# Performance work log

Measured on AMD Instinct MI355X. Metric: run time of the kernel, lower is better.

## Reference

```python
import jax, jax.numpy as jnp
import numpy as np

B, N, D = 16, 1369, 1024
HID, NH = 512, 8
SCALE = np.sqrt(D // NH)


def _pos_encoding_2d(n, d):
    ps = int(np.sqrt(n))  # 37; n is a perfect square here
    div = jnp.exp(jnp.arange(0, d // 2, 2, dtype=jnp.float32) * (-np.log(10000.0) / (d // 2)))
    rows = (jnp.arange(n) // ps).astype(jnp.float32)
    cols = (jnp.arange(n) % ps).astype(jnp.float32)
    def interleave(s, c):
        return jnp.stack([s, c], axis=-1).reshape(n, -1)
    half_row = interleave(jnp.sin(rows[:, None] * div), jnp.cos(rows[:, None] * div))
    half_col = interleave(jnp.sin(cols[:, None] * div), jnp.cos(cols[:, None] * div))
    return jnp.concatenate([half_row, half_col], axis=-1)  # [n, d]


def _center_bias(n, strength=0.3):
    ps = int(np.sqrt(n))
    c = ps // 2
    y, x = jnp.meshgrid(jnp.arange(ps, dtype=jnp.float32), jnp.arange(ps, dtype=jnp.float32), indexing='ij')
    d2 = (x - c) ** 2 + (y - c) ** 2
    sigma = ps / 6.0
    return (jnp.exp(-d2 / (2.0 * sigma ** 2)).reshape(-1)) * strength  # [n]


def setup_inputs() -> dict:
    key = jax.random.key(0)
    ks = jax.random.split(key, 16)
    s = 0.02
    return {
        'patch_tokens': jax.random.normal(ks[0], (B, N, D), dtype=jnp.float32),
        'curiosity_score': jax.random.uniform(ks[1], (B,), dtype=jnp.float32),
        'Wq': jax.random.normal(ks[2], (D, D), dtype=jnp.float32) * s,
        'bq': jax.random.uniform(ks[3], (D,), minval=-0.05, maxval=0.05, dtype=jnp.float32),
        'Wk': jax.random.normal(ks[4], (D, D), dtype=jnp.float32) * s,
        'bk': jax.random.uniform(ks[5], (D,), minval=-0.05, maxval=0.05, dtype=jnp.float32),
        'Wv': jax.random.normal(ks[6], (D, D), dtype=jnp.float32) * s,
        'bv': jnp.zeros((D,), dtype=jnp.float32),
        'Wc1': jax.random.normal(ks[7], (1, HID // 8), dtype=jnp.float32) * s,
        'bc1': jnp.zeros((HID // 8,), dtype=jnp.float32),
        'Wc2': jax.random.normal(ks[8], (HID // 8, NH), dtype=jnp.float32) * s,
        'bc2': jnp.zeros((NH,), dtype=jnp.float32),
        'Wp1': jax.random.normal(ks[9], (D, HID), dtype=jnp.float32) * s,
        'bp1': jnp.zeros((HID,), dtype=jnp.float32),
        'Wp2': jax.random.normal(ks[10], (HID, HID // 4), dtype=jnp.float32) * s,
        'bp2': jnp.zeros((HID // 4,), dtype=jnp.float32),
        'adaptive_weight': jnp.float32(0.5),
    }


def reference(patch_tokens, curiosity_score, Wq, bq, Wk, bk, Wv, bv,
              Wc1, bc1, Wc2, bc2, Wp1, bp1, Wp2, bp2, adaptive_weight):
    b, n, d = patch_tokens.shape
    x = patch_tokens + _pos_encoding_2d(n, d)[None]  # [B,N,D]

    q = x @ Wq + bq
    k = x @ Wk + bk
    v = x @ Wv + bv

    scores = jnp.einsum('bqd,bkd->bqk', q, k) / SCALE          # [B,N,N]
    attn = jax.nn.softmax(scores, axis=-1)                     # dropout p=0 / eval
    attended = jnp.einsum('bqk,bkd->bqd', attn, v)             # [B,N,D]

    cb = _center_bias(n)[None]                                 # [1,N]
    VAR_EPS = 1e-6

    pa = attn.mean(axis=1) + cb
    # fallback chain (data-dependent in torch; expressed with jnp.where)
    pa2 = jnp.diagonal(attn, axis1=-2, axis2=-1) + cb
    pa = jnp.where(jnp.var(pa, ddof=1) < VAR_EPS, pa2, pa)
    pa3 = attn.max(axis=-1) + cb
    pa = jnp.where(jnp.var(pa, ddof=1) < VAR_EPS, pa3, pa)
    norms = jnp.linalg.norm(x, axis=-1)
    noise = jax.random.normal(jax.random.key(42), norms.shape, dtype=norms.dtype) * 0.1 * jnp.std(norms, ddof=1)
    pa = jnp.where(jnp.var(pa, ddof=1) < VAR_EPS, norms + noise, pa)

    pa = pa / (pa.sum(axis=-1, keepdims=True) + 1e-8)

    # curiosity modulation
    h = jax.nn.relu(curiosity_score[:, None] @ Wc1 + bc1)
    cm = jax.nn.sigmoid(h @ Wc2 + bc2)                         # [B,NH]
    cw = cm.mean(axis=-1, keepdims=True)                       # [B,1]
    modulated = pa * (1.0 + cw)
    fa = adaptive_weight * modulated + (1.0 - adaptive_weight) * pa

    fa = jnp.clip(fa, 1e-8, None)
    fa = fa / (fa.sum(axis=-1, keepdims=True) + 1e-8)

    weighted = jnp.sum(attended * fa[..., None], axis=1)       # [B,D]
    focal = jax.nn.relu(weighted @ Wp1 + bp1) @ Wp2 + bp2      # [B,HID//4]
    return focal, fa
```

## Files before the change

kernel.cpp:

```cpp
#include <hip/hip_runtime.h>
#include <hip/hip_bf16.h>
#include <cstdint>

#define B_   16
#define N_   1369
#define NP   1408
#define D_   1024

typedef __bf16 bf16x8_t __attribute__((ext_vector_type(8)));
typedef __bf16 bf16x4_t __attribute__((ext_vector_type(4)));
typedef float  f32x4_t  __attribute__((ext_vector_type(4)));

__device__ __forceinline__ float  bf2f(__bf16 x) { return (float)x; }
__device__ __forceinline__ __bf16 f2bf(float x)  { return (__bf16)x; }

#define GLOAD_LDS16(g, l) __builtin_amdgcn_global_load_lds( \
    (const __attribute__((address_space(1))) void*)(g),     \
    (__attribute__((address_space(3))) void*)(l), 16, 0, 0)

__global__ __launch_bounds__(256)
void pos_kernel(float* __restrict__ pos)
{
    const int idx = blockIdx.x * 256 + threadIdx.x;
    if (idx >= N_ * D_) return;
    const int n = idx >> 10, f = idx & 1023;
    const int row = n / 37, col = n - row * 37;
    const float base = (f < 512) ? (float)row : (float)col;
    const int  t2   = (f & 511) >> 1;
    const float dv  = __expf(-0.03597789207803197f * (float)t2);
    const float ang = base * dv;
    pos[idx] = (f & 1) ? cosf(ang) : sinf(ang);
}

__global__ __launch_bounds__(256)
void addpos_kernel(const float* __restrict__ patch, const float* __restrict__ pos,
                   __bf16* __restrict__ X)
{
    const long tid = (long)blockIdx.x * 256 + threadIdx.x;
    const long e   = tid * 4;
    const int  f   = (int)(e & 1023);
    const long nb  = e >> 10;
    const int  n   = (int)(nb % NP);
    const long b   = nb / NP;
    bf16x4_t o;
    if (n < N_) {
        const float4 p = *(const float4*)(patch + ((b * N_ + n) << 10) + f);
        const float4 q = *(const float4*)(pos + ((long)n << 10) + f);
        o[0] = f2bf(p.x + q.x); o[1] = f2bf(p.y + q.y);
        o[2] = f2bf(p.z + q.z); o[3] = f2bf(p.w + q.w);
    } else {
        o[0] = o[1] = o[2] = o[3] = f2bf(0.f);
    }
    *(bf16x4_t*)(X + e) = o;
}

__global__ __launch_bounds__(256)
void wcast_kernel(const float* __restrict__ W0, const float* __restrict__ W1,
                  const float* __restrict__ W2,
                  __bf16* __restrict__ T0, __bf16* __restrict__ T1, __bf16* __restrict__ T2)
{
    const float* W = blockIdx.z == 0 ? W0 : (blockIdx.z == 1 ? W1 : W2);
    __bf16*      T = blockIdx.z == 0 ? T0 : (blockIdx.z == 1 ? T1 : T2);
    __shared__ float tile[64][65];
    const int o0 = blockIdx.x * 64, i0 = blockIdx.y * 64;
    const int t = threadIdx.x;
    const int tr = t >> 4, tc = (t & 15) * 4;
    #pragma unroll
    for (int rr = 0; rr < 64; rr += 16) {
        float4 v = *(const float4*)(W + (long)(i0 + rr + tr) * 1024 + o0 + tc);
        tile[rr + tr][tc + 0] = v.x; tile[rr + tr][tc + 1] = v.y;
        tile[rr + tr][tc + 2] = v.z; tile[rr + tr][tc + 3] = v.w;
    }
    __syncthreads();
    #pragma unroll
    for (int rr = 0; rr < 64; rr += 16) {
        bf16x4_t o;
        o[0] = f2bf(tile[tc + 0][rr + tr]); o[1] = f2bf(tile[tc + 1][rr + tr]);
        o[2] = f2bf(tile[tc + 2][rr + tr]); o[3] = f2bf(tile[tc + 3][rr + tr]);
        *(bf16x4_t*)(T + (long)(o0 + rr + tr) * 1024 + i0 + tc) = o;
    }
}

template<int HAS_BIAS>
__global__ __launch_bounds__(256)
void gemm_tn(const __bf16* __restrict__ A, const __bf16* __restrict__ Bt,
             __bf16* __restrict__ C, const float* __restrict__ bias,
             int M, int Nn, int Kd, float scale,
             long sA, long sB, long sC)
{
    A  += (long)blockIdx.z * sA;
    Bt += (long)blockIdx.z * sB;
    C  += (long)blockIdx.z * sC;
    const int m0 = blockIdx.y * 128;
    const int n0 = blockIdx.x * 128;
    __shared__ __bf16 As[128 * 32];
    __shared__ __bf16 Bs[128 * 32];
    const int t = threadIdx.x;
    const int w = t >> 6, l = t & 63;
    const int wr = w >> 1, wc = w & 1;
    const int lr = l & 15, lh = l >> 4;

    f32x4_t acc[4][4] = {};

    const __bf16* aRd = As + (wr * 64 + lr) * 32 + lh * 8;
    const __bf16* bRd = Bs + (wc * 64 + lr) * 32 + lh * 8;

    const int L0 = w * 1024 + l * 16;
    const int r0 = L0 >> 6;
    const int e0 = (L0 & 63) >> 1;
    const __bf16* gA0 = A  + (long)(m0 + r0)      * Kd + e0;
    const __bf16* gA1 = A  + (long)(m0 + r0 + 64) * Kd + e0;
    const __bf16* gB0 = Bt + (long)(n0 + r0)      * Kd + e0;
    const __bf16* gB1 = Bt + (long)(n0 + r0 + 64) * Kd + e0;
    __bf16* lA0 = As + w * 512;
    __bf16* lA1 = As + 2048 + w * 512;
    __bf16* lB0 = Bs + w * 512;
    __bf16* lB1 = Bs + 2048 + w * 512;

    for (int k0 = 0; k0 < Kd; k0 += 32) {
        GLOAD_LDS16(gA0 + k0, lA0);
        GLOAD_LDS16(gA1 + k0, lA1);
        GLOAD_LDS16(gB0 + k0, lB0);
        GLOAD_LDS16(gB1 + k0, lB1);
        __syncthreads();
        bf16x8_t af[4], bfm[4];
        #pragma unroll
        for (int i = 0; i < 4; ++i) af[i]  = *(const bf16x8_t*)(aRd + i * 16 * 32);
        #pragma unroll
        for (int j = 0; j < 4; ++j) bfm[j] = *(const bf16x8_t*)(bRd + j * 16 * 32);
        #pragma unroll
        for (int i = 0; i < 4; ++i)
            #pragma unroll
            for (int j = 0; j < 4; ++j)
                acc[i][j] = __builtin_amdgcn_mfma_f32_16x16x32_bf16(af[i], bfm[j], acc[i][j], 0, 0, 0);
        __syncthreads();
    }

    #pragma unroll
    for (int i = 0; i < 4; ++i) {
        const int row = m0 + wr * 64 + i * 16 + lh * 4;
        #pragma unroll
        for (int j = 0; j < 4; ++j) {
            const int col = n0 + wc * 64 + j * 16 + lr;
            const float bb = HAS_BIAS ? bias[col] : 0.0f;
            #pragma unroll
            for (int q = 0; q < 4; ++q) {
                const float v = acc[i][j][q] * scale + bb;
                C[(long)(row + q) * Nn + col] = f2bf(v);
            }
        }
    }
}

__global__ __launch_bounds__(256)
void softmax_kernel(__bf16* __restrict__ S)
{
    const int q = blockIdx.x, b = blockIdx.y;
    __bf16* row = S + ((long)b * NP + q) * NP;
    const int t = threadIdx.x;
    float v[6];
    float m = -1e30f;
    #pragma unroll
    for (int i = 0; i < 6; ++i) {
        const int k = t + i * 256;
        float x = -1e30f;
        if (k < N_) x = bf2f(row[k]);
        v[i] = x;
        m = fmaxf(m, x);
    }
    __shared__ float red[8];
    #pragma unroll
    for (int o = 32; o; o >>= 1) m = fmaxf(m, __shfl_xor(m, o));
    if (!(t & 63)) red[t >> 6] = m;
    __syncthreads();
    m = fmaxf(fmaxf(red[0], red[1]), fmaxf(red[2], red[3]));
    float s = 0.f;
    #pragma unroll
    for (int i = 0; i < 6; ++i) {
        const int k = t + i * 256;
        if (k < N_) { const float e = __expf(v[i] - m); v[i] = e; s += e; }
    }
    #pragma unroll
    for (int o = 32; o; o >>= 1) s += __shfl_xor(s, o);
    if (!(t & 63)) red[4 + (t >> 6)] = s;
    __syncthreads();
    s = red[4] + red[5] + red[6] + red[7];
    const float inv = 1.f / s;
    #pragma unroll
    for (int i = 0; i < 6; ++i) {
        const int k = t + i * 256;
        if (k < N_)      row[k] = f2bf(v[i] * inv);
        else if (k < NP) row[k] = f2bf(0.f);
    }
}

template<int WEIGHTED>
__global__ __launch_bounds__(256)
void colsum_kernel(const __bf16* __restrict__ attn, const float* __restrict__ wv,
                   float* __restrict__ out)
{
    const int k = blockIdx.x * 256 + threadIdx.x;
    const int b = blockIdx.y;
    const int q0 = blockIdx.z * 172;
    const int q1 = (q0 + 172 < N_) ? q0 + 172 : N_;
    if (k >= N_) return;
    const __bf16* base = attn + (long)b * NP * NP + k;
    float s = 0.f;
    for (int q = q0; q < q1; ++q) {
        float a = bf2f(base[(long)q * NP]);
        if (WEIGHTED) a *= wv[b * NP + q];
        s += a;
    }
    atomicAdd(out + b * NP + k, s);
}

__global__ __launch_bounds__(256)
void fa_kernel(const float* __restrict__ pa_raw, const float* __restrict__ curiosity,
               const float* __restrict__ Wc1, const float* __restrict__ bc1,
               const float* __restrict__ Wc2, const float* __restrict__ bc2,
               const float* __restrict__ aw_p,
               float* __restrict__ fa_ws, float* __restrict__ out_fa)
{
    const int b = blockIdx.x, t = threadIdx.x;
    __shared__ float hsh[64];
    __shared__ float red[8];
    __shared__ float cwsh;
    if (t < 64) hsh[t] = fmaxf(0.f, curiosity[b] * Wc1[t] + bc1[t]);
    __syncthreads();
    if (t < 8) {
        float a = bc2[t];
        for (int j = 0; j < 64; ++j) a += hsh[j] * Wc2[j * 8 + t];
        red[t] = 1.f / (1.f + __expf(-a));
    }
    __syncthreads();
    if (t == 0) {
        float cw = 0.f;
        for (int i = 0; i < 8; ++i) cw += red[i];
        cwsh = cw * 0.125f;
    }
    __syncthreads();
    const float aw   = aw_p[0];
    const float modf = 1.f + aw * cwsh;
    const float sig  = 37.f / 6.f;
    const float inv2s2 = 1.f / (2.f * sig * sig);
    float pv[6];
    float s1 = 0.f;
    #pragma unroll
    for (int i = 0; i < 6; ++i) {
        const int k = t + i * 256;
        float p = 0.f;
        if (k < N_) {
            const int y = k / 37, x = k - y * 37;
            const float d2 = (float)((x - 18) * (x - 18) + (y - 18) * (y - 18));
            const float cb = 0.3f * __expf(-d2 * inv2s2);
            p = pa_raw[b * NP + k] * (1.f / 1369.f) + cb;
        }
        pv[i] = p; s1 += p;
    }
    #pragma unroll
    for (int o = 32; o; o >>= 1) s1 += __shfl_xor(s1, o);
    __syncthreads();
    if (!(t & 63)) red[t >> 6] = s1;
    __syncthreads();
    s1 = red[0] + red[1] + red[2] + red[3];
    const float inv1 = 1.f / (s1 + 1e-8f);
    float s2 = 0.f;
    #pragma unroll
    for (int i = 0; i < 6; ++i) {
        const int k = t + i * 256;
        if (k < N_) {
            const float f = fmaxf(pv[i] * inv1 * modf, 1e-8f);
            pv[i] = f; s2 += f;
        }
    }
    #pragma unroll
    for (int o = 32; o; o >>= 1) s2 += __shfl_xor(s2, o);
    if (!(t & 63)) red[4 + (t >> 6)] = s2;
    __syncthreads();
    s2 = red[4] + red[5] + red[6] + red[7];
    const float inv2 = 1.f / (s2 + 1e-8f);
    #pragma unroll
    for (int i = 0; i < 6; ++i) {
        const int k = t + i * 256;
        if (k < N_) {
            const float f = pv[i] * inv2;
            fa_ws[b * NP + k]  = f;
            out_fa[b * N_ + k] = f;
        }
    }
}

__global__ __launch_bounds__(256)
void weighted_kernel(const float* __restrict__ g, const __bf16* __restrict__ V,
                     float* __restrict__ wout)
{
    const int b  = blockIdx.y;
    const int k0 = blockIdx.x * 86;
    const int k1 = (k0 + 86 < N_) ? k0 + 86 : N_;
    const int d  = threadIdx.x * 4;
    float a0 = 0, a1 = 0, a2 = 0, a3 = 0;
    const __bf16* vb = V + (long)b * NP * D_ + d;
    for (int k = k0; k < k1; ++k) {
        const float gv = g[b * NP + k];
        bf16x4_t vv = *(const bf16x4_t*)(vb + (long)k * D_);
        a0 += gv * bf2f(vv[0]); a1 += gv * bf2f(vv[1]);
        a2 += gv * bf2f(vv[2]); a3 += gv * bf2f(vv[3]);
    }
    atomicAdd(wout + b * D_ + d + 0, a0);
    atomicAdd(wout + b * D_ + d + 1, a1);
    atomicAdd(wout + b * D_ + d + 2, a2);
    atomicAdd(wout + b * D_ + d + 3, a3);
}

__global__ __launch_bounds__(256)
void focal_kernel(const float* __restrict__ weighted, const float* __restrict__ Wp1,
                  const float* __restrict__ bp1, const float* __restrict__ Wp2,
                  const float* __restrict__ bp2, float* __restrict__ out)
{
    const int b = blockIdx.x, t = threadIdx.x;
    __shared__ float wsh[1024];
    __shared__ float hsh[512];
    for (int i = t; i < 1024; i += 256) wsh[i] = weighted[b * 1024 + i];
    __syncthreads();
    for (int j = t; j < 512; j += 256) {
        float a = bp1[j];
        for (int d2 = 0; d2 < 1024; ++d2) a += wsh[d2] * Wp1[d2 * 512 + j];
        hsh[j] = fmaxf(a, 0.f);
    }
    __syncthreads();
    for (int o = t; o < 128; o += 256) {
        float a = bp2[o];
        for (int j = 0; j < 512; ++j) a += hsh[j] * Wp2[j * 128 + o];
        out[b * 128 + o] = a;
    }
}

extern "C" void kernel_launch(void* const* d_in, const int* in_sizes, int n_in,
                              void* d_out, int out_size, void* d_ws, size_t ws_size,
                              hipStream_t stream)
{
    const float* patch     = (const float*)d_in[0];
    const float* curiosity = (const float*)d_in[1];
    const float* Wq  = (const float*)d_in[2];
    const float* bq  = (const float*)d_in[3];
    const float* Wk  = (const float*)d_in[4];
    const float* bk  = (const float*)d_in[5];
    const float* Wv  = (const float*)d_in[6];
    const float* bv  = (const float*)d_in[7];
    const float* Wc1 = (const float*)d_in[8];
    const float* bc1 = (const float*)d_in[9];
    const float* Wc2 = (const float*)d_in[10];
    const float* bc2 = (const float*)d_in[11];
    const float* Wp1 = (const float*)d_in[12];
    const float* bp1 = (const float*)d_in[13];
    const float* Wp2 = (const float*)d_in[14];
    const float* bp2 = (const float*)d_in[15];
    const float* aw  = (const float*)d_in[16];
    float* out = (float*)d_out;

    char* ws = (char*)d_ws;
    size_t off = 0;
    auto alloc = [&](size_t bytes) -> char* {
        char* p = ws + off;
        off += (bytes + 255) & ~(size_t)255;
        return p;
    };
    float*  pos  = (float*) alloc((size_t)N_ * D_ * 4);
    __bf16* X    = (__bf16*)alloc((size_t)B_ * NP * D_ * 2);
    __bf16* WqT  = (__bf16*)alloc((size_t)D_ * D_ * 2);
    __bf16* WkT  = (__bf16*)alloc((size_t)D_ * D_ * 2);
    __bf16* WvT  = (__bf16*)alloc((size_t)D_ * D_ * 2);
    __bf16* Q    = (__bf16*)alloc((size_t)B_ * NP * D_ * 2);
    __bf16* Kb   = (__bf16*)alloc((size_t)B_ * NP * D_ * 2);
    __bf16* V    = (__bf16*)alloc((size_t)B_ * NP * D_ * 2);
    __bf16* S    = (__bf16*)alloc((size_t)B_ * NP * NP * 2);
    float*  pa   = (float*) alloc((size_t)B_ * NP * 4);
    float*  faw  = (float*) alloc((size_t)B_ * NP * 4);
    float*  gbuf = (float*) alloc((size_t)B_ * NP * 4);
    float*  wsum = (float*) alloc((size_t)B_ * D_ * 4);

    (void)hipMemsetAsync(pa,   0, (size_t)B_ * NP * 4, stream);
    (void)hipMemsetAsync(gbuf, 0, (size_t)B_ * NP * 4, stream);
    (void)hipMemsetAsync(wsum, 0, (size_t)B_ * D_ * 4, stream);

    pos_kernel<<<(N_ * D_ + 255) / 256, 256, 0, stream>>>(pos);
    addpos_kernel<<<(int)((size_t)B_ * NP * D_ / 4 / 256), 256, 0, stream>>>(patch, pos, X);
    {
        dim3 g(16, 16, 3);
        wcast_kernel<<<g, 256, 0, stream>>>(Wq, Wk, Wv, WqT, WkT, WvT);
    }
    {
        dim3 g(D_ / 128, (B_ * NP) / 128, 1);
        gemm_tn<1><<<g, 256, 0, stream>>>(X, WqT, Q,  bq, B_ * NP, D_, D_, 1.f, 0, 0, 0);
        gemm_tn<1><<<g, 256, 0, stream>>>(X, WkT, Kb, bk, B_ * NP, D_, D_, 1.f, 0, 0, 0);
        gemm_tn<1><<<g, 256, 0, stream>>>(X, WvT, V,  bv, B_ * NP, D_, D_, 1.f, 0, 0, 0);
    }
    {
        dim3 g(NP / 128, NP / 128, B_);
        gemm_tn<0><<<g, 256, 0, stream>>>(Q, Kb, S, nullptr, NP, NP, D_,
                                          0.08838834764831845f,
                                          (long)NP * D_, (long)NP * D_, (long)NP * NP);
    }
    {
        dim3 g(N_, B_);
        softmax_kernel<<<g, 256, 0, stream>>>(S);
    }
    {
        dim3 g(6, B_, 8);
        colsum_kernel<0><<<g, 256, 0, stream>>>(S, nullptr, pa);
    }
    fa_kernel<<<B_, 256, 0, stream>>>(pa, curiosity, Wc1, bc1, Wc2, bc2, aw,
                                      faw, out + B_ * 128);
    {
        dim3 g(6, B_, 8);
        colsum_kernel<1><<<g, 256, 0, stream>>>(S, faw, gbuf);
    }
    {
        dim3 g(16, B_);
        weighted_kernel<<<g, 256, 0, stream>>>(gbuf, V, wsum);
    }
    focal_kernel<<<B_, 256, 0, stream>>>(wsum, Wp1, bp1, Wp2, bp2, out);
}
```

Baseline: 639.6 us.

## Fuse QKV projections into one 256x256 pipelined MFMA GEMM with swizzled LDS

```diff
diff --git a/kernel.cpp b/kernel.cpp
--- a/kernel.cpp
+++ b/kernel.cpp
@@ -4,8 +4,9 @@
 
 #define B_   16
 #define N_   1369
-#define NP   1408
+#define NP   1536
 #define D_   1024
+#define NQKV 3072
 
 typedef __bf16 bf16x8_t __attribute__((ext_vector_type(8)));
 typedef __bf16 bf16x4_t __attribute__((ext_vector_type(4)));
@@ -81,75 +82,125 @@
     }
 }
 
+__global__ __launch_bounds__(256)
+void bcat_kernel(const float* __restrict__ bq, const float* __restrict__ bk,
+                 const float* __restrict__ bv, float* __restrict__ bcat)
+{
+    const int i = blockIdx.x * 256 + threadIdx.x;
+    if (i >= NQKV) return;
+    const int p = i >> 10, j = i & 1023;
+    bcat[i] = p == 0 ? bq[j] : (p == 1 ? bk[j] : bv[j]);
+}
+
 template<int HAS_BIAS>
-__global__ __launch_bounds__(256)
-void gemm_tn(const __bf16* __restrict__ A, const __bf16* __restrict__ Bt,
+__global__ __launch_bounds__(512, 2)
+void gemm256(const __bf16* __restrict__ A, const __bf16* __restrict__ Bt,
              __bf16* __restrict__ C, const float* __restrict__ bias,
-             int M, int Nn, int Kd, float scale,
-             long sA, long sB, long sC)
-{
-    A  += (long)blockIdx.z * sA;
-    Bt += (long)blockIdx.z * sB;
-    C  += (long)blockIdx.z * sC;
-    const int m0 = blockIdx.y * 128;
-    const int n0 = blockIdx.x * 128;
-    __shared__ __bf16 As[128 * 32];
-    __shared__ __bf16 Bs[128 * 32];
-    const int t = threadIdx.x;
-    const int w = t >> 6, l = t & 63;
-    const int wr = w >> 1, wc = w & 1;
+             int lda, int ldb, int ldc, int Kd, float scale,
+             long sA, long sB, long sC, int tilesN, int tilesPerBatch, int cpx)
+{
+    __shared__ __bf16 lds[65536];
+    const int bid = blockIdx.x;
+    const int vt  = (bid & 7) * cpx + (bid >> 3);
+    const int bz  = vt / tilesPerBatch;
+    const int rem = vt - bz * tilesPerBatch;
+    const int ty  = rem / tilesN;
+    const int tx  = rem - ty * tilesN;
+    A  += (long)bz * sA;  Bt += (long)bz * sB;  C += (long)bz * sC;
+    const int m0 = ty * 256, n0 = tx * 256;
+
+    const int t  = threadIdx.x;
+    const int w  = t >> 6, l = t & 63;
+    const int wr = w >> 2, wc = w & 3;
     const int lr = l & 15, lh = l >> 4;
 
-    f32x4_t acc[4][4] = {};
-
-    const __bf16* aRd = As + (wr * 64 + lr) * 32 + lh * 8;
-    const __bf16* bRd = Bs + (wc * 64 + lr) * 32 + lh * 8;
-
-    const int L0 = w * 1024 + l * 16;
-    const int r0 = L0 >> 6;
-    const int e0 = (L0 & 63) >> 1;
-    const __bf16* gA0 = A  + (long)(m0 + r0)      * Kd + e0;
-    const __bf16* gA1 = A  + (long)(m0 + r0 + 64) * Kd + e0;
-    const __bf16* gB0 = Bt + (long)(n0 + r0)      * Kd + e0;
-    const __bf16* gB1 = Bt + (long)(n0 + r0 + 64) * Kd + e0;
-    __bf16* lA0 = As + w * 512;
-    __bf16* lA1 = As + 2048 + w * 512;
-    __bf16* lB0 = Bs + w * 512;
-    __bf16* lB1 = Bs + 2048 + w * 512;
-
-    for (int k0 = 0; k0 < Kd; k0 += 32) {
-        GLOAD_LDS16(gA0 + k0, lA0);
-        GLOAD_LDS16(gA1 + k0, lA1);
-        GLOAD_LDS16(gB0 + k0, lB0);
-        GLOAD_LDS16(gB1 + k0, lB1);
-        __syncthreads();
-        bf16x8_t af[4], bfm[4];
+    const int laneF  = (lr * 64 + ((lh * 16) ^ (((lr >> 3) & 1) << 5))) >> 1;
+    const int rstage = w * 16 + (l >> 2);
+    const int kstage = ((l & 3) * 8) ^ (((l >> 5) & 1) << 4);
+
+    const __bf16* Ag = A  + (long)(m0 + rstage) * lda + kstage;
+    const __bf16* Bg = Bt + (long)(n0 + rstage) * ldb + kstage;
+    __bf16* dA = lds + (w * 2) * 512;
+    __bf16* dB = lds + 16384 + (w * 2) * 512;
+
+#define SA_(buf, half, kt) do {                                       \
+    const __bf16* g_ = Ag + (long)(half) * 128 * lda + (kt) * 64;     \
+    __bf16* d_ = dA + (buf) * 32768 + (half) * 8192;                  \
+    GLOAD_LDS16(g_, d_); GLOAD_LDS16(g_ + 32, d_ + 512); } while (0)
+#define SB_(buf, half, kt) do {                                       \
+    const __bf16* g_ = Bg + (long)(half) * 128 * ldb + (kt) * 64;     \
+    __bf16* d_ = dB + (buf) * 32768 + (half) * 8192;                  \
+    GLOAD_LDS16(g_, d_); GLOAD_LDS16(g_ + 32, d_ + 512); } while (0)
+
+    f32x4_t acc[8][4] = {};
+    bf16x8_t bfr[4][2];
+
+#define BREADS_() do { const __bf16* bp_ = lds + cbB + laneF;                              \
+    bfr[0][0] = *(const bf16x8_t*)(bp_);        bfr[0][1] = *(const bf16x8_t*)(bp_ + 512); \
+    bfr[1][0] = *(const bf16x8_t*)(bp_ + 1024); bfr[1][1] = *(const bf16x8_t*)(bp_ + 1536);\
+    bfr[2][0] = *(const bf16x8_t*)(bp_ + 2048); bfr[2][1] = *(const bf16x8_t*)(bp_ + 2560);\
+    bfr[3][0] = *(const bf16x8_t*)(bp_ + 3072); bfr[3][1] = *(const bf16x8_t*)(bp_ + 3584);} while (0)
+
+#define PHASE_(p, P0R, STG, VMW) do {                                                  \
+    const __bf16* ap_ = lds + cbase + wr * 8192 + (p) * 2048 + laneF;                  \
+    bf16x8_t a00 = *(const bf16x8_t*)(ap_);                                            \
+    bf16x8_t a01 = *(const bf16x8_t*)(ap_ + 512);                                      \
+    bf16x8_t a10 = *(const bf16x8_t*)(ap_ + 1024);                                     \
+    bf16x8_t a11 = *(const bf16x8_t*)(ap_ + 1536);                                     \
+    P0R;                                                                               \
+    STG;                                                                               \
+    __builtin_amdgcn_s_barrier();                                                      \
+    asm volatile("s_waitcnt lgkmcnt(0)" ::: "memory");                                 \
+    __builtin_amdgcn_sched_barrier(0);                                                 \
+    __builtin_amdgcn_s_setprio(1);                                                     \
+    _Pragma("unroll") for (int nn = 0; nn < 4; ++nn)                                   \
+      acc[(p)*2+0][nn] = __builtin_amdgcn_mfma_f32_16x16x32_bf16(a00, bfr[nn][0], acc[(p)*2+0][nn], 0, 0, 0); \
+    _Pragma("unroll") for (int nn = 0; nn < 4; ++nn)                                   \
+      acc[(p)*2+1][nn] = __builtin_amdgcn_mfma_f32_16x16x32_bf16(a10, bfr[nn][0], acc[(p)*2+1][nn], 0, 0, 0); \
+    _Pragma("unroll") for (int nn = 0; nn < 4; ++nn)                                   \
+      acc[(p)*2+0][nn] = __builtin_amdgcn_mfma_f32_16x16x32_bf16(a01, bfr[nn][1], acc[(p)*2+0][nn], 0, 0, 0); \
+    _Pragma("unroll") for (int nn = 0; nn < 4; ++nn)                                   \
+      acc[(p)*2+1][nn] = __builtin_amdgcn_mfma_f32_16x16x32_bf16(a11, bfr[nn][1], acc[(p)*2+1][nn], 0, 0, 0); \
+    __builtin_amdgcn_s_setprio(0);                                                     \
+    VMW;                                                                               \
+    __builtin_amdgcn_s_barrier();                                                      \
+  } while (0)
+
+    const int NT = Kd >> 6;
+    SA_(0, 0, 0); SA_(0, 1, 0); SB_(0, 0, 0); SB_(0, 1, 0);
+    SB_(1, 0, 1); SB_(1, 1, 1);
+    asm volatile("s_waitcnt vmcnt(4)" ::: "memory");
+    __builtin_amdgcn_s_barrier();
+
+    for (int tk = 0; tk < NT; ++tk) {
+        const int c  = tk & 1, o = c ^ 1;
+        const int t1 = (tk + 1 < NT) ? tk + 1 : NT - 1;
+        const int t2 = (tk + 2 < NT) ? tk + 2 : NT - 1;
+        const int cbase = c * 32768;
+        const int cbB   = cbase + 16384 + wc * 4096;
+        PHASE_(0, BREADS_(), SA_(o, 0, t1), ((void)0));
+        PHASE_(1, ((void)0), SA_(o, 1, t1), ((void)0));
+        PHASE_(2, ((void)0), SB_(c, 0, t2), ((void)0));
+        PHASE_(3, ((void)0), SB_(c, 1, t2),
+               asm volatile("s_waitcnt vmcnt(4)" ::: "memory"));
+    }
+
+    #pragma unroll
+    for (int mi = 0; mi < 8; ++mi) {
+        const int row = m0 + wr * 128 + mi * 16 + lh * 4;
         #pragma unroll
-        for (int i = 0; i < 4; ++i) af[i]  = *(const bf16x8_t*)(aRd + i * 16 * 32);
-        #pragma unroll
-        for (int j = 0; j < 4; ++j) bfm[j] = *(const bf16x8_t*)(bRd + j * 16 * 32);
-        #pragma unroll
-        for (int i = 0; i < 4; ++i)
-            #pragma unroll
-            for (int j = 0; j < 4; ++j)
-                acc[i][j] = __builtin_amdgcn_mfma_f32_16x16x32_bf16(af[i], bfm[j], acc[i][j], 0, 0, 0);
-        __syncthreads();
-    }
-
-    #pragma unroll
-    for (int i = 0; i < 4; ++i) {
-        const int row = m0 + wr * 64 + i * 16 + lh * 4;
-        #pragma unroll
-        for (int j = 0; j < 4; ++j) {
-            const int col = n0 + wc * 64 + j * 16 + lr;
+        for (int nn = 0; nn < 4; ++nn) {
+            const int col = n0 + wc * 64 + nn * 16 + lr;
             const float bb = HAS_BIAS ? bias[col] : 0.0f;
             #pragma unroll
-            for (int q = 0; q < 4; ++q) {
-                const float v = acc[i][j][q] * scale + bb;
-                C[(long)(row + q) * Nn + col] = f2bf(v);
-            }
+            for (int q = 0; q < 4; ++q)
+                C[(long)(row + q) * ldc + col] = f2bf(acc[mi][nn][q] * scale + bb);
         }
     }
+#undef SA_
+#undef SB_
+#undef BREADS_
+#undef PHASE_
 }
 
 __global__ __launch_bounds__(256)
@@ -190,7 +241,7 @@
     for (int i = 0; i < 6; ++i) {
         const int k = t + i * 256;
         if (k < N_)      row[k] = f2bf(v[i] * inv);
-        else if (k < NP) row[k] = f2bf(0.f);
+        else             row[k] = f2bf(0.f);
     }
 }
 
@@ -292,17 +343,17 @@
 
 __global__ __launch_bounds__(256)
 void weighted_kernel(const float* __restrict__ g, const __bf16* __restrict__ V,
-                     float* __restrict__ wout)
+                     int ldv, float* __restrict__ wout)
 {
     const int b  = blockIdx.y;
     const int k0 = blockIdx.x * 86;
     const int k1 = (k0 + 86 < N_) ? k0 + 86 : N_;
     const int d  = threadIdx.x * 4;
     float a0 = 0, a1 = 0, a2 = 0, a3 = 0;
-    const __bf16* vb = V + (long)b * NP * D_ + d;
+    const __bf16* vb = V + (long)b * NP * ldv + d;
     for (int k = k0; k < k1; ++k) {
         const float gv = g[b * NP + k];
-        bf16x4_t vv = *(const bf16x4_t*)(vb + (long)k * D_);
+        bf16x4_t vv = *(const bf16x4_t*)(vb + (long)k * ldv);
         a0 += gv * bf2f(vv[0]); a1 += gv * bf2f(vv[1]);
         a2 += gv * bf2f(vv[2]); a3 += gv * bf2f(vv[3]);
     }
@@ -367,17 +418,16 @@
     };
     float*  pos  = (float*) alloc((size_t)N_ * D_ * 4);
     __bf16* X    = (__bf16*)alloc((size_t)B_ * NP * D_ * 2);
-    __bf16* WqT  = (__bf16*)alloc((size_t)D_ * D_ * 2);
-    __bf16* WkT  = (__bf16*)alloc((size_t)D_ * D_ * 2);
-    __bf16* WvT  = (__bf16*)alloc((size_t)D_ * D_ * 2);
-    __bf16* Q    = (__bf16*)alloc((size_t)B_ * NP * D_ * 2);
-    __bf16* Kb   = (__bf16*)alloc((size_t)B_ * NP * D_ * 2);
-    __bf16* V    = (__bf16*)alloc((size_t)B_ * NP * D_ * 2);
-    __bf16* S    = (__bf16*)alloc((size_t)B_ * NP * NP * 2);
+    __bf16* WT   = (__bf16*)alloc((size_t)3 * D_ * D_ * 2);
+    const size_t S_BYTES = (size_t)B_ * NP * NP * 2;
+    if (off < S_BYTES) off = S_BYTES;
+    __bf16* S    = (__bf16*)ws;
+    __bf16* QKV  = (__bf16*)alloc((size_t)B_ * NP * NQKV * 2);
     float*  pa   = (float*) alloc((size_t)B_ * NP * 4);
     float*  faw  = (float*) alloc((size_t)B_ * NP * 4);
     float*  gbuf = (float*) alloc((size_t)B_ * NP * 4);
     float*  wsum = (float*) alloc((size_t)B_ * D_ * 4);
+    float*  bcat = (float*) alloc((size_t)NQKV * 4);
 
     (void)hipMemsetAsync(pa,   0, (size_t)B_ * NP * 4, stream);
     (void)hipMemsetAsync(gbuf, 0, (size_t)B_ * NP * 4, stream);
@@ -387,19 +437,23 @@
     addpos_kernel<<<(int)((size_t)B_ * NP * D_ / 4 / 256), 256, 0, stream>>>(patch, pos, X);
     {
         dim3 g(16, 16, 3);
-        wcast_kernel<<<g, 256, 0, stream>>>(Wq, Wk, Wv, WqT, WkT, WvT);
-    }
-    {
-        dim3 g(D_ / 128, (B_ * NP) / 128, 1);
-        gemm_tn<1><<<g, 256, 0, stream>>>(X, WqT, Q,  bq, B_ * NP, D_, D_, 1.f, 0, 0, 0);
-        gemm_tn<1><<<g, 256, 0, stream>>>(X, WkT, Kb, bk, B_ * NP, D_, D_, 1.f, 0, 0, 0);
-        gemm_tn<1><<<g, 256, 0, stream>>>(X, WvT, V,  bv, B_ * NP, D_, D_, 1.f, 0, 0, 0);
-    }
-    {
-        dim3 g(NP / 128, NP / 128, B_);
-        gemm_tn<0><<<g, 256, 0, stream>>>(Q, Kb, S, nullptr, NP, NP, D_,
-                                          0.08838834764831845f,
-                                          (long)NP * D_, (long)NP * D_, (long)NP * NP);
+        wcast_kernel<<<g, 256, 0, stream>>>(Wq, Wk, Wv,
+                                            WT, WT + D_ * D_, WT + 2 * D_ * D_);
+    }
+    bcat_kernel<<<(NQKV + 255) / 256, 256, 0, stream>>>(bq, bk, bv, bcat);
+    {
+        const int nwg = 96 * 12;
+        gemm256<1><<<nwg, 512, 0, stream>>>(X, WT, QKV, bcat,
+                                            D_, D_, NQKV, D_, 1.0f,
+                                            0, 0, 0, 12, nwg, nwg / 8);
+    }
+    {
+        const int nwg = 36 * B_;
+        gemm256<0><<<nwg, 512, 0, stream>>>(QKV, QKV + D_, S, nullptr,
+                                            NQKV, NQKV, NP, D_,
+                                            0.08838834764831845f,
+                                            (long)NP * NQKV, (long)NP * NQKV,
+                                            (long)NP * NP, 6, 36, nwg / 8);
     }
     {
         dim3 g(N_, B_);
@@ -417,7 +471,7 @@
     }
     {
         dim3 g(16, B_);
-        weighted_kernel<<<g, 256, 0, stream>>>(gbuf, V, wsum);
+        weighted_kernel<<<g, 256, 0, stream>>>(gbuf, QKV + 2 * D_, NQKV, wsum);
     }
     focal_kernel<<<B_, 256, 0, stream>>>(wsum, Wp1, bp1, Wp2, bp2, out);
 }
```

Result: faster. 537.0 us (-16.0%).
